# Optimization experiments

Measured on AMD Instinct MI355X. Metric: run time of the kernel, lower is better.

## Reference

```python
import jax, jax.numpy as jnp
import numpy as np

B, L, D, H, UNITS = 64, 4096, 512, 512, 256

def setup_inputs() -> dict:
    key = jax.random.key(0)
    ks = jax.random.split(key, 8)
    s = lambda fan_in: 1.0 / np.sqrt(fan_in)
    return {
        "features": jax.random.normal(ks[0], (B, L, D), dtype=jnp.float32),
        "hidden": jax.random.normal(ks[1], (B, H), dtype=jnp.float32),
        "W1_k": jax.random.uniform(ks[2], (D, UNITS), jnp.float32, -s(D), s(D)),
        "W1_b": jnp.zeros((UNITS,), jnp.float32),
        "W2_k": jax.random.uniform(ks[3], (H, UNITS), jnp.float32, -s(H), s(H)),
        "W2_b": jnp.zeros((UNITS,), jnp.float32),
        "V_k": jax.random.uniform(ks[4], (UNITS, 1), jnp.float32, -s(UNITS), s(UNITS)),
        "V_b": jnp.zeros((1,), jnp.float32),
    }

def reference(features, hidden, W1_k, W1_b, W2_k, W2_b, V_k, V_b):
    # features: [B, L, D], hidden: [B, H]
    f_proj = jnp.einsum('bld,du->blu', features, W1_k) + W1_b          # [B, L, U]
    h_proj = (hidden @ W2_k + W2_b)[:, None, :]                        # [B, 1, U]
    score = jnp.einsum('blu,uo->blo', jnp.tanh(f_proj + h_proj), V_k) + V_b  # [B, L, 1]
    attention_weights = jax.nn.softmax(score, axis=1)                  # [B, L, 1]
    context_vector = jnp.sum(attention_weights * features, axis=1)     # [B, D]
    return (context_vector, attention_weights)
```

## Files before the change

### kernel.cpp

```cpp
#include <hip/hip_runtime.h>

#define Bsz 64
#define Lsz 4096
#define Dsz 512
#define Hsz 512
#define Usz 256
#define LT  64
#define NLB (Lsz / LT)
#define AW  520

typedef __attribute__((ext_vector_type(8))) short s8v;
typedef __attribute__((ext_vector_type(4))) float f4v;
typedef __attribute__((ext_vector_type(8))) unsigned short u16x8;

__device__ __forceinline__ unsigned short f2bf(float f) {
    unsigned int u = __float_as_uint(f);
    u += 0x7FFFu + ((u >> 16) & 1u);
    return (unsigned short)(u >> 16);
}
__device__ __forceinline__ float bf2f(unsigned int lo16) {
    return __uint_as_float(lo16 << 16);
}
__device__ __forceinline__ void barrier_lds() {
    asm volatile("s_waitcnt lgkmcnt(0)" ::: "memory");
    __builtin_amdgcn_s_barrier();
}


__global__ __launch_bounds__(256) void k_prep(const float* __restrict__ W1,
                                              const float* __restrict__ hidden,
                                              const float* __restrict__ W2,
                                              unsigned short* __restrict__ W1T,
                                              float* __restrict__ hp_part,
                                              float* __restrict__ den,
                                              float* __restrict__ ctx_acc) {
    int blk = blockIdx.x, tid = threadIdx.x;
    if (blk < 32) {
        __shared__ unsigned short Lt[64][72];
        int kb = blk >> 2, ub = blk & 3;
        {
            int rr = tid >> 2, c16 = (tid & 3) * 16;
            const float* src = W1 + (size_t)(kb * 64 + rr) * Usz + ub * 64 + c16;
            f4v v0 = *reinterpret_cast<const f4v*>(src);
            f4v v1 = *reinterpret_cast<const f4v*>(src + 4);
            f4v v2 = *reinterpret_cast<const f4v*>(src + 8);
            f4v v3 = *reinterpret_cast<const f4v*>(src + 12);
            u16x8 o0 = { f2bf(v0.x), f2bf(v0.y), f2bf(v0.z), f2bf(v0.w),
                         f2bf(v1.x), f2bf(v1.y), f2bf(v1.z), f2bf(v1.w) };
            u16x8 o1 = { f2bf(v2.x), f2bf(v2.y), f2bf(v2.z), f2bf(v2.w),
                         f2bf(v3.x), f2bf(v3.y), f2bf(v3.z), f2bf(v3.w) };
            *reinterpret_cast<u16x8*>(&Lt[rr][c16])     = o0;
            *reinterpret_cast<u16x8*>(&Lt[rr][c16 + 8]) = o1;
        }
        __syncthreads();
        {
            int ur = tid >> 2, k16 = (tid & 3) * 16;
            u16x8 o0, o1;
#pragma unroll
            for (int i = 0; i < 8; ++i) o0[i] = Lt[k16 + i][ur];
#pragma unroll
            for (int i = 0; i < 8; ++i) o1[i] = Lt[k16 + 8 + i][ur];
            unsigned short* dst = W1T + (size_t)(ub * 64 + ur) * Dsz + kb * 64 + k16;
            *reinterpret_cast<u16x8*>(dst)     = o0;
            *reinterpret_cast<u16x8*>(dst + 8) = o1;
        }
    } else if (blk < 288) {
        int idx = blk - 32;
        int kq = idx >> 6, b = idx & 63;
        const float* hrow = hidden + (size_t)b * Hsz + kq * 128;
        const float* w2p  = W2 + (size_t)(kq * 128) * Usz + tid;
        float a0 = 0.f, a1 = 0.f, a2 = 0.f, a3 = 0.f;
#pragma unroll 8
        for (int k = 0; k < 128; k += 4) {
            a0 = fmaf(hrow[k + 0], w2p[(size_t)(k + 0) * Usz], a0);
            a1 = fmaf(hrow[k + 1], w2p[(size_t)(k + 1) * Usz], a1);
            a2 = fmaf(hrow[k + 2], w2p[(size_t)(k + 2) * Usz], a2);
            a3 = fmaf(hrow[k + 3], w2p[(size_t)(k + 3) * Usz], a3);
        }
        hp_part[((size_t)kq * Bsz + b) * Usz + tid] = (a0 + a1) + (a2 + a3);
    } else {
        int b = blk - 288;
        if (tid == 0) den[b] = 0.f;
        ctx_acc[b * Dsz + tid] = 0.f;
        ctx_acc[b * Dsz + 256 + tid] = 0.f;
    }
}

__global__ void __launch_bounds__(512)
__attribute__((amdgpu_waves_per_eu(4, 4))) k_score_ctx(
    const float* __restrict__ feat, const unsigned short* __restrict__ W1T,
    const float* __restrict__ hp_part, const float* __restrict__ W1b,
    const float* __restrict__ W2b, const float* __restrict__ Vk,
    const float* __restrict__ Vb, float* __restrict__ el_arr,
    float* __restrict__ den, float* __restrict__ ctx_acc)
{
    __shared__ __align__(16) unsigned short A[LT][AW];
    __shared__ float hp[Usz], vv[Usz];
    __shared__ float spart[8][LT];
    __shared__ float el[LT];
    __shared__ float pc[2][Dsz];

    const int tid  = threadIdx.x;
    const int w    = tid >> 6;
    const int lane = tid & 63;
    const int lr   = lane & 15;
    const int lg   = lane >> 4;
    const int b    = blockIdx.x >> 6;
    const int lb   = blockIdx.x & 63;
    const int l0   = lb * LT;

    const int srow = tid >> 3;
    const int scol = (tid & 7) * 16;
    const float* fb = feat + ((size_t)b * Lsz + l0) * Dsz + (size_t)srow * Dsz + scol;

    f4v st[4];
#pragma unroll
    for (int i = 0; i < 4; ++i) st[i] = *reinterpret_cast<const f4v*>(fb + i * 4);

    if (tid < Usz) {
        const float* hpb = hp_part + (size_t)b * Usz + tid;
        hp[tid] = (hpb[0] + hpb[Bsz * Usz]) + (hpb[2 * Bsz * Usz] + hpb[3 * Bsz * Usz])
                + W1b[tid] + W2b[tid];
        vv[tid] = Vk[tid];
    }
    {
        u16x8 o0 = { f2bf(st[0].x), f2bf(st[0].y), f2bf(st[0].z), f2bf(st[0].w),
                     f2bf(st[1].x), f2bf(st[1].y), f2bf(st[1].z), f2bf(st[1].w) };
        u16x8 o1 = { f2bf(st[2].x), f2bf(st[2].y), f2bf(st[2].z), f2bf(st[2].w),
                     f2bf(st[3].x), f2bf(st[3].y), f2bf(st[3].z), f2bf(st[3].w) };
        *reinterpret_cast<u16x8*>(&A[srow][scol])     = o0;
        *reinterpret_cast<u16x8*>(&A[srow][scol + 8]) = o1;
    }
    __syncthreads();

    const unsigned short* bp0 = W1T + (size_t)(w * 32 + lr) * Dsz + lg * 8;
    const unsigned short* bp1 = bp0 + 16 * Dsz;
    f4v acc[4][2];
#pragma unroll
    for (int mf = 0; mf < 4; ++mf) {
        acc[mf][0] = (f4v){0.f, 0.f, 0.f, 0.f};
        acc[mf][1] = (f4v){0.f, 0.f, 0.f, 0.f};
    }

#pragma unroll
    for (int c = 0; c < 4; ++c) {
        s8v bq[4][2];
#pragma unroll
        for (int k = 0; k < 4; ++k) {
            bq[k][0] = *reinterpret_cast<const s8v*>(bp0 + (c * 4 + k) * 32);
            bq[k][1] = *reinterpret_cast<const s8v*>(bp1 + (c * 4 + k) * 32);
        }
        __builtin_amdgcn_sched_barrier(0);
        if (c < 3) {
#pragma unroll
            for (int i = 0; i < 4; ++i)
                st[i] = *reinterpret_cast<const f4v*>(fb + (c + 1) * 128 + i * 4);
        }
        __builtin_amdgcn_sched_barrier(0);
#pragma unroll
        for (int k = 0; k < 4; ++k) {
            const int kof = (c * 4 + k) * 32 + lg * 8;
#pragma unroll
            for (int mf = 0; mf < 4; ++mf) {
                s8v a = *reinterpret_cast<const s8v*>(&A[mf * 16 + lr][kof]);
                acc[mf][0] = __builtin_amdgcn_mfma_f32_16x16x32_bf16(a, bq[k][0], acc[mf][0], 0, 0, 0);
                acc[mf][1] = __builtin_amdgcn_mfma_f32_16x16x32_bf16(a, bq[k][1], acc[mf][1], 0, 0, 0);
            }
        }
        __builtin_amdgcn_sched_barrier(0);
        if (c < 3) {
            const int cc = (c + 1) * 128 + scol;
            u16x8 o0 = { f2bf(st[0].x), f2bf(st[0].y), f2bf(st[0].z), f2bf(st[0].w),
                         f2bf(st[1].x), f2bf(st[1].y), f2bf(st[1].z), f2bf(st[1].w) };
            u16x8 o1 = { f2bf(st[2].x), f2bf(st[2].y), f2bf(st[2].z), f2bf(st[2].w),
                         f2bf(st[3].x), f2bf(st[3].y), f2bf(st[3].z), f2bf(st[3].w) };
            *reinterpret_cast<u16x8*>(&A[srow][cc])     = o0;
            *reinterpret_cast<u16x8*>(&A[srow][cc + 8]) = o1;
            barrier_lds();
        }
    }

    {
        float rs[4][4];
#pragma unroll
        for (int mf = 0; mf < 4; ++mf)
#pragma unroll
            for (int r = 0; r < 4; ++r) rs[mf][r] = 0.f;
#pragma unroll
        for (int mf = 0; mf < 4; ++mf)
#pragma unroll
            for (int nf = 0; nf < 2; ++nf) {
                int col = w * 32 + nf * 16 + lr;
                float hpv = hp[col], vvv = vv[col];
#pragma unroll
                for (int r = 0; r < 4; ++r) {
                    float x = acc[mf][nf][r] + hpv;
                    float e = __expf(2.f * x);
                    rs[mf][r] = fmaf(1.f - 2.f / (e + 1.f), vvv, rs[mf][r]);
                }
            }
#pragma unroll
        for (int off = 1; off < 16; off <<= 1)
#pragma unroll
            for (int mf = 0; mf < 4; ++mf)
#pragma unroll
                for (int r = 0; r < 4; ++r)
                    rs[mf][r] += __shfl_xor(rs[mf][r], off, 64);
        if (lr == 0)
#pragma unroll
            for (int mf = 0; mf < 4; ++mf)
#pragma unroll
                for (int r = 0; r < 4; ++r)
                    spart[w][mf * 16 + lg * 4 + r] = rs[mf][r];
    }
    __syncthreads();

    if (tid < LT) {
        float s = Vb[0];
#pragma unroll
        for (int ww = 0; ww < 8; ++ww) s += spart[ww][tid];
        float e = __expf(s);
        el[tid] = e;
        el_arr[(size_t)b * Lsz + l0 + tid] = e;
        float es = e;
#pragma unroll
        for (int off = 1; off < 64; off <<= 1) es += __shfl_xor(es, off, 64);
        if (tid == 0) atomicAdd(&den[b], es);
    }
    __syncthreads();

    {
        const int qr = tid >> 8;
        const int d0 = (tid & 255) * 2;
        float a0 = 0.f, a1 = 0.f;
#pragma unroll 8
        for (int li = 0; li < 32; ++li) {
            int l = qr * 32 + li;
            unsigned int pk = *reinterpret_cast<const unsigned int*>(&A[l][d0]);
            float e = el[l];
            a0 = fmaf(e, bf2f(pk & 0xFFFFu), a0);
            a1 = fmaf(e, bf2f(pk >> 16), a1);
        }
        pc[qr][d0]     = a0;
        pc[qr][d0 + 1] = a1;
    }
    __syncthreads();
    atomicAdd(&ctx_acc[b * Dsz + tid], pc[0][tid] + pc[1][tid]);
}

__global__ __launch_bounds__(256) void k_finalize(const float* __restrict__ el_arr,
                                                  const float* __restrict__ den,
                                                  const float* __restrict__ ctx_acc,
                                                  float* __restrict__ ctx,
                                                  float* __restrict__ wout) {
    int blk = blockIdx.x, tid = threadIdx.x;
    int b = blk >> 2, q = blk & 3;
    float inv = 1.f / den[b];
    size_t base = (size_t)b * Lsz + q * 1024 + tid * 4;
    f4v e4 = *reinterpret_cast<const f4v*>(&el_arr[base]);
    f4v w4 = { e4.x * inv, e4.y * inv, e4.z * inv, e4.w * inv };
    *reinterpret_cast<f4v*>(&wout[base]) = w4;
    if (tid < 128) {
        int d = q * 128 + tid;
        ctx[(size_t)b * Dsz + d] = ctx_acc[b * Dsz + d] * inv;
    }
}

extern "C" void kernel_launch(void* const* d_in, const int* in_sizes, int n_in,
                              void* d_out, int out_size, void* d_ws, size_t ws_size,
                              hipStream_t stream) {
    const float* feat   = (const float*)d_in[0];
    const float* hidden = (const float*)d_in[1];
    const float* W1     = (const float*)d_in[2];
    const float* W1b    = (const float*)d_in[3];
    const float* W2     = (const float*)d_in[4];
    const float* W2b    = (const float*)d_in[5];
    const float* Vk     = (const float*)d_in[6];
    const float* Vb     = (const float*)d_in[7];

    unsigned short* w1t = (unsigned short*)d_ws;
    float* hp_part = (float*)((char*)d_ws + 256 * 1024);
    float* el_arr  = (float*)((char*)d_ws + 512 * 1024);
    float* den     = (float*)((char*)d_ws + 1536 * 1024);
    float* ctx_acc = (float*)((char*)d_ws + 1536 * 1024 + 256);

    float* ctx  = (float*)d_out;
    float* wout = ctx + Bsz * Dsz;

    k_prep<<<352, 256, 0, stream>>>(W1, hidden, W2, w1t, hp_part, den, ctx_acc);
    k_score_ctx<<<Bsz * NLB, 512, 0, stream>>>(feat, w1t, hp_part, W1b, W2b,
                                               Vk, Vb, el_arr, den, ctx_acc);
    k_finalize<<<Bsz * 4, 256, 0, stream>>>(el_arr, den, ctx_acc, ctx, wout);
}
```

Measured before the change: 190.6 us.

## Swizzle LDS feature tile and double-buffer global prefetch two chunks ahead

Replaces the padded LDS row stride (520) with an unpadded 512-wide tile addressed through an XOR swizzle on 8-element groups, which reduces LDS footprint and is meant to avoid bank conflicts on the MFMA A-fragment reads. It also adds a second register staging buffer so feature loads are issued two K-chunks ahead instead of one, hiding more global latency at the cost of extra VGPRs. Several __syncthreads calls are replaced with a lightweight lgkmcnt wait plus s_barrier. Risks include register pressure under the fixed 4-waves-per-EU bound and the weaker barrier missing pending global memory ordering.

```diff
diff --git a/kernel.cpp b/kernel.cpp
--- a/kernel.cpp
+++ b/kernel.cpp
@@ -7,11 +7,12 @@
 #define Usz 256
 #define LT  64
 #define NLB (Lsz / LT)
-#define AW  520
 
 typedef __attribute__((ext_vector_type(8))) short s8v;
 typedef __attribute__((ext_vector_type(4))) float f4v;
 typedef __attribute__((ext_vector_type(8))) unsigned short u16x8;
+
+#define SW(r, c) (((((c) >> 3) ^ ((r) & 7)) << 3) | ((c) & 7))
 
 __device__ __forceinline__ unsigned short f2bf(float f) {
     unsigned int u = __float_as_uint(f);
@@ -94,7 +95,7 @@
     const float* __restrict__ Vb, float* __restrict__ el_arr,
     float* __restrict__ den, float* __restrict__ ctx_acc)
 {
-    __shared__ __align__(16) unsigned short A[LT][AW];
+    __shared__ __align__(16) unsigned short A[LT][Dsz];
     __shared__ float hp[Usz], vv[Usz];
     __shared__ float spart[8][LT];
     __shared__ float el[LT];
@@ -110,12 +111,15 @@
     const int l0   = lb * LT;
 
     const int srow = tid >> 3;
-    const int scol = (tid & 7) * 16;
-    const float* fb = feat + ((size_t)b * Lsz + l0) * Dsz + (size_t)srow * Dsz + scol;
-
-    f4v st[4];
-#pragma unroll
-    for (int i = 0; i < 4; ++i) st[i] = *reinterpret_cast<const f4v*>(fb + i * 4);
+    const int sfc  = (tid & 7) * 16;
+    const float* fb = feat + ((size_t)b * Lsz + l0 + srow) * Dsz + sfc;
+
+    f4v st[2][4];
+#pragma unroll
+    for (int i = 0; i < 4; ++i) st[0][i] = *reinterpret_cast<const f4v*>(fb + i * 4);
+#pragma unroll
+    for (int i = 0; i < 4; ++i) st[1][i] = *reinterpret_cast<const f4v*>(fb + 128 + i * 4);
+    __builtin_amdgcn_sched_barrier(0);
 
     if (tid < Usz) {
         const float* hpb = hp_part + (size_t)b * Usz + tid;
@@ -124,14 +128,14 @@
         vv[tid] = Vk[tid];
     }
     {
-        u16x8 o0 = { f2bf(st[0].x), f2bf(st[0].y), f2bf(st[0].z), f2bf(st[0].w),
-                     f2bf(st[1].x), f2bf(st[1].y), f2bf(st[1].z), f2bf(st[1].w) };
-        u16x8 o1 = { f2bf(st[2].x), f2bf(st[2].y), f2bf(st[2].z), f2bf(st[2].w),
-                     f2bf(st[3].x), f2bf(st[3].y), f2bf(st[3].z), f2bf(st[3].w) };
-        *reinterpret_cast<u16x8*>(&A[srow][scol])     = o0;
-        *reinterpret_cast<u16x8*>(&A[srow][scol + 8]) = o1;
-    }
-    __syncthreads();
+        u16x8 o0 = { f2bf(st[0][0].x), f2bf(st[0][0].y), f2bf(st[0][0].z), f2bf(st[0][0].w),
+                     f2bf(st[0][1].x), f2bf(st[0][1].y), f2bf(st[0][1].z), f2bf(st[0][1].w) };
+        u16x8 o1 = { f2bf(st[0][2].x), f2bf(st[0][2].y), f2bf(st[0][2].z), f2bf(st[0][2].w),
+                     f2bf(st[0][3].x), f2bf(st[0][3].y), f2bf(st[0][3].z), f2bf(st[0][3].w) };
+        *reinterpret_cast<u16x8*>(&A[srow][SW(srow, sfc)])     = o0;
+        *reinterpret_cast<u16x8*>(&A[srow][SW(srow, sfc + 8)]) = o1;
+    }
+    barrier_lds();
 
     const unsigned short* bp0 = W1T + (size_t)(w * 32 + lr) * Dsz + lg * 8;
     const unsigned short* bp1 = bp0 + 16 * Dsz;
@@ -151,10 +155,10 @@
             bq[k][1] = *reinterpret_cast<const s8v*>(bp1 + (c * 4 + k) * 32);
         }
         __builtin_amdgcn_sched_barrier(0);
-        if (c < 3) {
+        if (c < 2) {
 #pragma unroll
             for (int i = 0; i < 4; ++i)
-                st[i] = *reinterpret_cast<const f4v*>(fb + (c + 1) * 128 + i * 4);
+                st[c & 1][i] = *reinterpret_cast<const f4v*>(fb + (c + 2) * 128 + i * 4);
         }
         __builtin_amdgcn_sched_barrier(0);
 #pragma unroll
@@ -162,20 +166,22 @@
             const int kof = (c * 4 + k) * 32 + lg * 8;
 #pragma unroll
             for (int mf = 0; mf < 4; ++mf) {
-                s8v a = *reinterpret_cast<const s8v*>(&A[mf * 16 + lr][kof]);
+                const int row = mf * 16 + lr;
+                s8v a = *reinterpret_cast<const s8v*>(&A[row][SW(row, kof)]);
                 acc[mf][0] = __builtin_amdgcn_mfma_f32_16x16x32_bf16(a, bq[k][0], acc[mf][0], 0, 0, 0);
                 acc[mf][1] = __builtin_amdgcn_mfma_f32_16x16x32_bf16(a, bq[k][1], acc[mf][1], 0, 0, 0);
             }
         }
         __builtin_amdgcn_sched_barrier(0);
         if (c < 3) {
-            const int cc = (c + 1) * 128 + scol;
-            u16x8 o0 = { f2bf(st[0].x), f2bf(st[0].y), f2bf(st[0].z), f2bf(st[0].w),
-                         f2bf(st[1].x), f2bf(st[1].y), f2bf(st[1].z), f2bf(st[1].w) };
-            u16x8 o1 = { f2bf(st[2].x), f2bf(st[2].y), f2bf(st[2].z), f2bf(st[2].w),
-                         f2bf(st[3].x), f2bf(st[3].y), f2bf(st[3].z), f2bf(st[3].w) };
-            *reinterpret_cast<u16x8*>(&A[srow][cc])     = o0;
-            *reinterpret_cast<u16x8*>(&A[srow][cc + 8]) = o1;
+            const int cc = (c + 1) * 128 + sfc;
+            const f4v* s = st[(c + 1) & 1];
+            u16x8 o0 = { f2bf(s[0].x), f2bf(s[0].y), f2bf(s[0].z), f2bf(s[0].w),
+                         f2bf(s[1].x), f2bf(s[1].y), f2bf(s[1].z), f2bf(s[1].w) };
+            u16x8 o1 = { f2bf(s[2].x), f2bf(s[2].y), f2bf(s[2].z), f2bf(s[2].w),
+                         f2bf(s[3].x), f2bf(s[3].y), f2bf(s[3].z), f2bf(s[3].w) };
+            *reinterpret_cast<u16x8*>(&A[srow][SW(srow, cc)])     = o0;
+            *reinterpret_cast<u16x8*>(&A[srow][SW(srow, cc + 8)]) = o1;
             barrier_lds();
         }
     }
@@ -213,7 +219,7 @@
                 for (int r = 0; r < 4; ++r)
                     spart[w][mf * 16 + lg * 4 + r] = rs[mf][r];
     }
-    __syncthreads();
+    barrier_lds();
 
     if (tid < LT) {
         float s = Vb[0];
@@ -227,7 +233,7 @@
         for (int off = 1; off < 64; off <<= 1) es += __shfl_xor(es, off, 64);
         if (tid == 0) atomicAdd(&den[b], es);
     }
-    __syncthreads();
+    barrier_lds();
 
     {
         const int qr = tid >> 8;
@@ -236,7 +242,7 @@
 #pragma unroll 8
         for (int li = 0; li < 32; ++li) {
             int l = qr * 32 + li;
-            unsigned int pk = *reinterpret_cast<const unsigned int*>(&A[l][d0]);
+            unsigned int pk = *reinterpret_cast<const unsigned int*>(&A[l][SW(l, d0)]);
             float e = el[l];
             a0 = fmaf(e, bf2f(pk & 0xFFFFu), a0);
             a1 = fmaf(e, bf2f(pk >> 16), a1);
@@ -244,7 +250,7 @@
         pc[qr][d0]     = a0;
         pc[qr][d0 + 1] = a1;
     }
-    __syncthreads();
+    barrier_lds();
     atomicAdd(&ctx_acc[b * Dsz + tid], pc[0][tid] + pc[1][tid]);
 }
 
```

Measured after the change: 194.6 us. +2.1%, slower.
